# Optimization experiments

Hardware: AMD Instinct MI355X
Metric: run time of the kernel (lower is better)

The kernel has to match this reference:

```python
import jax, jax.numpy as jnp
import numpy as np

B, V, NL, D, H, DH, FS, CD, TL = 16, 8192, 12, 1024, 16, 64, 16, 768, 128
INNER, FF, SEQ = H * DH, 4 * D, FS * FS - 1  # 1024, 4096, 255
EPS = 1e-5


def _pos_indices(size):
    ar = np.arange(size)
    pos = np.stack(np.meshgrid(ar, ar, indexing='ij'), -1).reshape(-1, 2)  # (size^2, 2)
    rel = pos[:, None, :] - pos[None, :, :] + size - 1
    return jnp.asarray(rel[..., 0] * (2 * size - 1) + rel[..., 1])  # (size^2, size^2)


POS_IDX = _pos_indices(FS)


def _ln(x, g):
    mu = jnp.mean(x, -1, keepdims=True)
    var = jnp.mean(jnp.square(x - mu), -1, keepdims=True)
    return (x - mu) * jax.lax.rsqrt(var + EPS) * g


def _attn(x, ctx, g, Wq, nullkv, Wkv, Wout, og, pos_bias=None, ctx_mask=None, causal=False):
    b, n = x.shape[0], x.shape[1]
    xn = _ln(x, g)
    if ctx is None:
        ctx = xn  # self-attention: context is the normed input
    q = (xn @ Wq).reshape(b, n, H, DH).transpose(0, 2, 1, 3) * DH ** -0.5  # [b,h,n,dh]
    kv = ctx @ Wkv  # multi-query: single shared kv head [b,m,dh]
    kv = jnp.concatenate([jnp.broadcast_to(nullkv, (b, 1, DH)), kv], axis=1)  # null kv
    j = kv.shape[1]
    sim = jnp.einsum('bhid,bjd->bhij', q, kv)
    if pos_bias is not None:
        bias = pos_bias[POS_IDX[:n, :j - 1]]  # [n, j-1, h]
        sim = sim + jnp.pad(jnp.transpose(bias, (2, 0, 1)), ((0, 0), (0, 0), (1, 0)))
    big = jnp.finfo(sim.dtype).max
    if ctx_mask is not None:
        m = jnp.concatenate([jnp.ones((b, 1), bool), ctx_mask], axis=1)  # null kv never masked
        sim = jnp.where(m[:, None, None, :], sim, -big)
    if causal:
        cm = jnp.triu(jnp.ones((n, j), bool), k=j - n + 1)
        sim = jnp.where(cm, -big, sim)
    attn = jax.nn.softmax(sim.astype(jnp.float32), axis=-1).astype(sim.dtype)
    out = jnp.einsum('bhij,bjd->bhid', attn, kv).transpose(0, 2, 1, 3).reshape(b, n, INNER)
    return _ln(out @ Wout, og)


def setup_inputs() -> dict:
    key = jax.random.key(0)
    ks = iter(jax.random.split(key, 40))
    r = lambda *s: jax.random.normal(next(ks), s, jnp.float32) * 0.02
    return dict(
        image_token_ids=jax.random.randint(next(ks), (B, SEQ), 0, V),
        text_token_embeds=jax.random.normal(next(ks), (B, TL, CD), jnp.float32),
        text_mask=jnp.ones((B, TL), bool),
        tok_emb=r(V, D),
        axial_height_pos=r(FS, D),
        axial_width_pos=r(FS, D),
        start_token=r(D),
        init_gamma=jnp.ones(D, jnp.float32),
        sa_norm_g=jnp.ones((NL, D), jnp.float32), sa_Wq=r(NL, D, INNER), sa_null=r(NL, DH),
        sa_Wkv=r(NL, D, DH), sa_Wout=r(NL, INNER, D), sa_out_g=jnp.ones((NL, D), jnp.float32),
        sa_posbias=r(NL, (2 * FS - 1) ** 2, H),
        ca_norm_g=jnp.ones((NL, D), jnp.float32), ca_Wq=r(NL, D, INNER), ca_null=r(NL, DH),
        ca_Wkv=r(NL, CD, DH), ca_Wout=r(NL, INNER, D), ca_out_g=jnp.ones((NL, D), jnp.float32),
        ff_g1=jnp.ones((NL, D), jnp.float32), ff_W1=r(NL, D, FF),
        ff_g2=jnp.ones((NL, FF), jnp.float32), ff_W2=r(NL, FF, D),
        final_gamma=jnp.ones(D, jnp.float32),
    )


def reference(image_token_ids, text_token_embeds, text_mask, tok_emb, axial_height_pos,
              axial_width_pos, start_token, init_gamma, sa_norm_g, sa_Wq, sa_null, sa_Wkv,
              sa_Wout, sa_out_g, sa_posbias, ca_norm_g, ca_Wq, ca_null, ca_Wkv, ca_Wout,
              ca_out_g, ff_g1, ff_W1, ff_g2, ff_W2, final_gamma):
    b = image_token_ids.shape[0]
    emb = tok_emb[image_token_ids]  # [b, 255, D]
    axial = (axial_height_pos[:, None, :] + axial_width_pos[None, :, :]).reshape(-1, D)
    emb = emb + axial[:emb.shape[1]]
    x = jnp.concatenate([jnp.broadcast_to(start_token, (b, 1, D)), emb], axis=1)  # [b,256,D]
    # cond_drop_prob = 0: text_mask used as-is (deterministic)
    x = _ln(x, init_gamma)
    for l in range(NL):
        x = _attn(x, None, sa_norm_g[l], sa_Wq[l], sa_null[l], sa_Wkv[l], sa_Wout[l],
                  sa_out_g[l], pos_bias=sa_posbias[l], causal=True) + x
        x = _attn(x, text_token_embeds, ca_norm_g[l], ca_Wq[l], ca_null[l], ca_Wkv[l],
                  ca_Wout[l], ca_out_g[l], ctx_mask=text_mask) + x
        h = jax.nn.gelu(_ln(x, ff_g1[l]) @ ff_W1[l], approximate=False)
        x = _ln(h, ff_g2[l]) @ ff_W2[l] + x
    x = _ln(x, final_gamma)
    return x @ tok_emb.T  # tied embedding logits [b,256,V]
```

## Files before the change

kernel.cpp:

```cpp
#include <hip/hip_runtime.h>
#include <math.h>

typedef unsigned short u16;
typedef __attribute__((ext_vector_type(4))) unsigned short u16x4;
typedef __attribute__((ext_vector_type(8))) unsigned short u16x8;
typedef __attribute__((ext_vector_type(8))) short s16x8;
typedef __attribute__((ext_vector_type(4))) float f32x4;

#define DEV __device__ __forceinline__

DEV u16 f2bf(float f) {
  unsigned u = __float_as_uint(f);
  u += 0x7fffu + ((u >> 16) & 1u);
  return (u16)(u >> 16);
}
DEV float bf2f(u16 h) { return __uint_as_float(((unsigned)h) << 16); }

DEV void gload_lds16(const u16* g, u16* l) {
  __builtin_amdgcn_global_load_lds(
      (const __attribute__((address_space(1))) unsigned int*)(const void*)g,
      (__attribute__((address_space(3))) unsigned int*)(void*)l, 16, 0, 0);
}

template<int N> DEV void wait_vm() {
  if constexpr (N == 8)      asm volatile("s_waitcnt vmcnt(8)" ::: "memory");
  else if constexpr (N == 6) asm volatile("s_waitcnt vmcnt(6)" ::: "memory");
  else if constexpr (N == 4) asm volatile("s_waitcnt vmcnt(4)" ::: "memory");
  else                       asm volatile("s_waitcnt vmcnt(0)" ::: "memory");
}

DEV float block_sum256(float v, float* sb) {
  #pragma unroll
  for (int o = 32; o > 0; o >>= 1) v += __shfl_down(v, o);
  __syncthreads();
  if ((threadIdx.x & 63) == 0) sb[threadIdx.x >> 6] = v;
  __syncthreads();
  return sb[0] + sb[1] + sb[2] + sb[3];
}

__global__ __launch_bounds__(256) void wconv_t(const float* __restrict__ in, u16* __restrict__ outp,
                                               int R, int C, size_t ils, size_t ols, float sc) {
  __shared__ float tile[32][33];
  const float* inl = in + (size_t)blockIdx.z * ils;
  u16* outl = outp + (size_t)blockIdx.z * ols;
  int r0 = blockIdx.x * 32, c0 = blockIdx.y * 32;
  int tx = threadIdx.x, ty = threadIdx.y;
  #pragma unroll
  for (int i = ty; i < 32; i += 8)
    tile[i][tx] = inl[(size_t)(r0 + i) * C + (c0 + tx)];
  __syncthreads();
  #pragma unroll
  for (int i = ty; i < 32; i += 8)
    outl[(size_t)(c0 + i) * R + (r0 + tx)] = f2bf(tile[tx][i] * sc);
}

__global__ __launch_bounds__(256) void cvt_bf16_kernel(const float* __restrict__ in, u16* __restrict__ outp, size_t n) {
  size_t i = (size_t)blockIdx.x * blockDim.x + threadIdx.x;
  size_t stride = (size_t)gridDim.x * blockDim.x;
  for (; i < n; i += stride) outp[i] = f2bf(in[i]);
}

__global__ __launch_bounds__(256) void zfill16(u16* __restrict__ p, size_t lstride) {
  size_t o = (size_t)blockIdx.y * lstride + ((size_t)blockIdx.x * 256 + threadIdx.x) * 8;
  *(u16x8*)(p + o) = (u16x8){0, 0, 0, 0, 0, 0, 0, 0};
}

__global__ __launch_bounds__(256) void bias_tr(const float* __restrict__ pb, float* __restrict__ bt) {
  int l = blockIdx.x;
  for (int idx = threadIdx.x; idx < 961 * 16; idx += 256) {
    int p = idx >> 4, h = idx & 15;
    bt[((size_t)l * 16 + h) * 961 + p] = pb[(size_t)l * 15376 + idx];
  }
}

template<int BM, int BN, int WM, int WN, bool OUTBF>
__global__ __launch_bounds__(512, 2)
void gemm8(const u16* __restrict__ A, const u16* __restrict__ Bt, void* __restrict__ Cout,
           int M, int N, int K, int KS) {
  constexpr int BK = 64;
  constexpr int WROWS = BM / WM, WCOLS = BN / WN;
  constexpr int MR = WROWS / 16, NR = WCOLS / 16;
  constexpr int ABYTES = BM * BK * 2, BBYTES = BN * BK * 2;
  constexpr int TBYTES = ABYTES + BBYTES;
  constexpr int NCHA = ABYTES / 8192, NCHB = BBYTES / 8192;
  constexpr int LOADS = NCHA + NCHB;
  __shared__ char lds[2 * TBYTES];
  const int tid = threadIdx.x;
  const int lane = tid & 63;
  const int wave = tid >> 6;
  const int wr = wave / WN, wc = wave % WN;
  const int gX = gridDim.x;
  const int nwg = gX * gridDim.y;
  const int orig = blockIdx.y * gX + blockIdx.x;
  const int lin = (orig & 7) * (nwg >> 3) + (orig >> 3);
  const int bx = lin % gX, by = lin / gX;
  const size_t m0 = (size_t)bx * BM, n0 = (size_t)by * BN;
  const int k0 = blockIdx.z * KS;
  const size_t ldb = (size_t)K * 2;
  const char* Ab = (const char*)A + m0 * ldb + (size_t)k0 * 2;
  const char* Bb = (const char*)Bt + n0 * ldb + (size_t)k0 * 2;
  const int NT = KS / BK;

  auto stage = [&](int kt, char* buf) {
    const char* ga = Ab + kt * (BK * 2);
    #pragma unroll
    for (int c = 0; c < NCHA; ++c) {
      int d = (tid + c * 512) * 16;
      int o = d ^ (((d >> 9) & 1) << 5);
      gload_lds16((const u16*)(ga + (size_t)(o >> 7) * ldb + (o & 127)), (u16*)(buf + d));
    }
    const char* gb = Bb + kt * (BK * 2);
    #pragma unroll
    for (int c = 0; c < NCHB; ++c) {
      int d = (tid + c * 512) * 16;
      int o = d ^ (((d >> 9) & 1) << 5);
      gload_lds16((const u16*)(gb + (size_t)(o >> 7) * ldb + (o & 127)), (u16*)(buf + ABYTES + d));
    }
  };

  stage(0, lds);
  stage(1, lds + TBYTES);

  f32x4 acc[MR][NR];
  #pragma unroll
  for (int i = 0; i < MR; ++i)
    #pragma unroll
    for (int j = 0; j < NR; ++j) acc[i][j] = (f32x4){0.f, 0.f, 0.f, 0.f};

  const int rlane = lane & 15;
  const int glane = lane >> 4;
  const int swz = ((lane >> 2) & 1) << 5;

  for (int kt = 0; kt < NT; ++kt) {
    char* buf = lds + (kt & 1) * TBYTES;
    const char* At = buf;
    const char* Btl = buf + ABYTES;
    if (kt + 1 < NT) wait_vm<LOADS>(); else wait_vm<0>();
    asm volatile("s_barrier" ::: "memory");
    s16x8 bfr[NR][2];
    #pragma unroll
    for (int j = 0; j < NR; ++j)
      #pragma unroll
      for (int ks = 0; ks < 2; ++ks) {
        int o = ((wc * WCOLS + j * 16 + rlane) * 128 + ks * 64 + glane * 16) ^ swz;
        bfr[j][ks] = *(const s16x8*)(Btl + o);
      }
    #pragma unroll
    for (int mh = 0; mh < 2; ++mh) {
      s16x8 af[MR / 2][2];
      #pragma unroll
      for (int i = 0; i < MR / 2; ++i)
        #pragma unroll
        for (int ks = 0; ks < 2; ++ks) {
          int row = wr * WROWS + (mh * (MR / 2) + i) * 16 + rlane;
          int o = (row * 128 + ks * 64 + glane * 16) ^ swz;
          af[i][ks] = *(const s16x8*)(At + o);
        }
      __builtin_amdgcn_s_setprio(1);
      #pragma unroll
      for (int i = 0; i < MR / 2; ++i)
        #pragma unroll
        for (int j = 0; j < NR; ++j)
          #pragma unroll
          for (int ks = 0; ks < 2; ++ks)
            acc[mh * (MR / 2) + i][j] = __builtin_amdgcn_mfma_f32_16x16x32_bf16(
                af[i][ks], bfr[j][ks], acc[mh * (MR / 2) + i][j], 0, 0, 0);
      __builtin_amdgcn_s_setprio(0);
    }
    asm volatile("s_waitcnt lgkmcnt(0)\n\ts_barrier" ::: "memory");
    if (kt + 2 < NT) stage(kt + 2, buf);
  }

  char* Cb = (char*)Cout + (size_t)blockIdx.z * M * (size_t)N * (OUTBF ? 2 : 4);
  #pragma unroll
  for (int i = 0; i < MR; ++i)
    #pragma unroll
    for (int j = 0; j < NR; ++j) {
      size_t row = m0 + wr * WROWS + i * 16 + glane * 4;
      size_t col = n0 + wc * WCOLS + j * 16 + rlane;
      #pragma unroll
      for (int r = 0; r < 4; ++r) {
        size_t off = (row + r) * (size_t)N + col;
        if (OUTBF) ((u16*)Cb)[off] = f2bf(acc[i][j][r]);
        else       ((float*)Cb)[off] = acc[i][j][r];
      }
    }
}

template<bool OUTBF>
__global__ __launch_bounds__(256) void ln1024(const float* __restrict__ X, const float* __restrict__ g,
                                              float* Of, u16* Ob) {
  __shared__ float sb[4];
  size_t row = blockIdx.x;
  f32x4 v = *(const f32x4*)(X + row * 1024 + threadIdx.x * 4);
  float s = v[0] + v[1] + v[2] + v[3];
  float mu = block_sum256(s, sb) * (1.f / 1024.f);
  float q = 0.f;
  #pragma unroll
  for (int c = 0; c < 4; ++c) { float d = v[c] - mu; q += d * d; }
  float var = block_sum256(q, sb) * (1.f / 1024.f);
  float rs = rsqrtf(var + 1e-5f);
  f32x4 gg = *(const f32x4*)(g + threadIdx.x * 4);
  if (OUTBF) {
    u16x4 o;
    #pragma unroll
    for (int c = 0; c < 4; ++c) o[c] = f2bf((v[c] - mu) * rs * gg[c]);
    *(u16x4*)(Ob + row * 1024 + threadIdx.x * 4) = o;
  } else {
    f32x4 o;
    #pragma unroll
    for (int c = 0; c < 4; ++c) o[c] = (v[c] - mu) * rs * gg[c];
    *(f32x4*)(Of + row * 1024 + threadIdx.x * 4) = o;
  }
}

__global__ __launch_bounds__(256) void lnln_kernel(const float* __restrict__ T, const float* __restrict__ og,
                                                   const float* __restrict__ X, const float* __restrict__ g2,
                                                   float* __restrict__ Xn, u16* __restrict__ Ob) {
  __shared__ float sb[4];
  size_t row = blockIdx.x;
  size_t o4 = row * 1024 + threadIdx.x * 4;
  f32x4 v = *(const f32x4*)(T + o4);
  float s = v[0] + v[1] + v[2] + v[3];
  float mu = block_sum256(s, sb) * (1.f / 1024.f);
  float q = 0.f;
  #pragma unroll
  for (int c = 0; c < 4; ++c) { float d = v[c] - mu; q += d * d; }
  float var = block_sum256(q, sb) * (1.f / 1024.f);
  float rs = rsqrtf(var + 1e-5f);
  f32x4 ogv = *(const f32x4*)(og + threadIdx.x * 4);
  f32x4 xv  = *(const f32x4*)(X + o4);
  f32x4 u;
  #pragma unroll
  for (int c = 0; c < 4; ++c) u[c] = (v[c] - mu) * rs * ogv[c] + xv[c];
  *(f32x4*)(Xn + o4) = u;
  float s2 = u[0] + u[1] + u[2] + u[3];
  float mu2 = block_sum256(s2, sb) * (1.f / 1024.f);
  float q2 = 0.f;
  #pragma unroll
  for (int c = 0; c < 4; ++c) { float d = u[c] - mu2; q2 += d * d; }
  float var2 = block_sum256(q2, sb) * (1.f / 1024.f);
  float rs2 = rsqrtf(var2 + 1e-5f);
  f32x4 g2v = *(const f32x4*)(g2 + threadIdx.x * 4);
  u16x4 ob;
  #pragma unroll
  for (int c = 0; c < 4; ++c) ob[c] = f2bf((u[c] - mu2) * rs2 * g2v[c]);
  *(u16x4*)(Ob + o4) = ob;
}

__global__ __launch_bounds__(256) void addln_kernel(const float* __restrict__ X, const float* __restrict__ P0,
                                                    const float* __restrict__ g,
                                                    float* __restrict__ Xn, u16* __restrict__ Ob) {
  __shared__ float sb[4];
  size_t row = blockIdx.x;
  size_t o4 = row * 1024 + threadIdx.x * 4;
  f32x4 a = *(const f32x4*)(X + o4);
  f32x4 p = *(const f32x4*)(P0 + o4);
  f32x4 v;
  #pragma unroll
  for (int c = 0; c < 4; ++c) v[c] = a[c] + p[c];
  *(f32x4*)(Xn + o4) = v;
  float s = v[0] + v[1] + v[2] + v[3];
  float mu = block_sum256(s, sb) * (1.f / 1024.f);
  float q = 0.f;
  #pragma unroll
  for (int c = 0; c < 4; ++c) { float d = v[c] - mu; q += d * d; }
  float var = block_sum256(q, sb) * (1.f / 1024.f);
  float rs = rsqrtf(var + 1e-5f);
  f32x4 gg = *(const f32x4*)(g + threadIdx.x * 4);
  u16x4 ob;
  #pragma unroll
  for (int c = 0; c < 4; ++c) ob[c] = f2bf((v[c] - mu) * rs * gg[c]);
  *(u16x4*)(Ob + o4) = ob;
}

__global__ __launch_bounds__(256) void gelu_ln_bf(const u16* __restrict__ T, const float* __restrict__ g,
                                                  u16* __restrict__ Ob) {
  __shared__ float sb[4];
  size_t row = blockIdx.x;
  size_t o16 = row * 4096 + threadIdx.x * 16;
  u16x8 t0 = *(const u16x8*)(T + o16);
  u16x8 t1 = *(const u16x8*)(T + o16 + 8);
  float v[16];
  #pragma unroll
  for (int c = 0; c < 8; ++c) {
    float a = bf2f(t0[c]);
    v[c] = 0.5f * a * (1.f + erff(a * 0.70710678118654752f));
    float b = bf2f(t1[c]);
    v[c + 8] = 0.5f * b * (1.f + erff(b * 0.70710678118654752f));
  }
  float s = 0.f;
  #pragma unroll
  for (int c = 0; c < 16; ++c) s += v[c];
  float mu = block_sum256(s, sb) * (1.f / 4096.f);
  float q = 0.f;
  #pragma unroll
  for (int c = 0; c < 16; ++c) { float d = v[c] - mu; q += d * d; }
  float var = block_sum256(q, sb) * (1.f / 4096.f);
  float rs = rsqrtf(var + 1e-5f);
  u16x8 o0, o1;
  #pragma unroll
  for (int c = 0; c < 8; ++c) {
    o0[c] = f2bf((v[c] - mu) * rs * g[threadIdx.x * 16 + c]);
    o1[c] = f2bf((v[c + 8] - mu) * rs * g[threadIdx.x * 16 + 8 + c]);
  }
  *(u16x8*)(Ob + o16) = o0;
  *(u16x8*)(Ob + o16 + 8) = o1;
}

__global__ __launch_bounds__(256) void embed_ln_kernel(const int* __restrict__ ids, const float* __restrict__ tok,
                                                       const float* __restrict__ hpos, const float* __restrict__ wpos,
                                                       const float* __restrict__ start, const float* __restrict__ gamma,
                                                       float* __restrict__ X) {
  __shared__ float sb[4];
  int p = blockIdx.x, b = blockIdx.y;
  float v[4];
  if (p == 0) {
    #pragma unroll
    for (int c = 0; c < 4; ++c) v[c] = start[threadIdx.x + c * 256];
  } else {
    int s = p - 1;
    int id = ids[b * 255 + s];
    #pragma unroll
    for (int c = 0; c < 4; ++c) {
      int col = threadIdx.x + c * 256;
      v[c] = tok[(size_t)id * 1024 + col] + hpos[(s >> 4) * 1024 + col] + wpos[(s & 15) * 1024 + col];
    }
  }
  float s0 = 0.f;
  #pragma unroll
  for (int c = 0; c < 4; ++c) s0 += v[c];
  float mu = block_sum256(s0, sb) * (1.f / 1024.f);
  float q = 0.f;
  #pragma unroll
  for (int c = 0; c < 4; ++c) { float d = v[c] - mu; q += d * d; }
  float var = block_sum256(q, sb) * (1.f / 1024.f);
  float rs = rsqrtf(var + 1e-5f);
  #pragma unroll
  for (int c = 0; c < 4; ++c) {
    int col = threadIdx.x + c * 256;
    X[((size_t)b * 256 + p) * 1024 + col] = (v[c] - mu) * rs * gamma[col];
  }
}

__global__ __launch_bounds__(256) void kv_build_sa(const u16* __restrict__ qkv, const float* __restrict__ nul,
                                                   u16* __restrict__ kv, u16* __restrict__ kvT) {
  constexpr int JP = 288, J = 257;
  int b = blockIdx.x;
  for (int idx = threadIdx.x; idx < JP * 64; idx += 256) {
    int j = idx >> 6, d = idx & 63;
    u16 hv = 0;
    if (j == 0) hv = f2bf(nul[d]);
    else if (j < J) hv = qkv[(size_t)(b * 256 + j - 1) * 1152 + 1024 + d];
    kv[((size_t)b * JP + j) * 64 + d] = hv;
    kvT[((size_t)b * 64 + d) * JP + j] = hv;
  }
}

__global__ __launch_bounds__(256) void kv_build_ca(const u16* __restrict__ src, int sstride, int scol,
                                                   const float* __restrict__ nul,
                                                   u16* __restrict__ kv, u16* __restrict__ kvT) {
  constexpr int JP = 160, J = 129;
  int b = blockIdx.x, l = blockIdx.y;
  for (int idx = threadIdx.x; idx < JP * 64; idx += 256) {
    int j = idx >> 6, d = idx & 63;
    u16 hv = 0;
    if (j == 0) hv = f2bf(nul[l * 64 + d]);
    else if (j < J) hv = src[(size_t)(b * 128 + j - 1) * sstride + l * scol + d];
    kv[(((size_t)l * 16 + b) * JP + j) * 64 + d] = hv;
    kvT[(((size_t)l * 16 + b) * 64 + d) * JP + j] = hv;
  }
}

template<int NJT, int KSP, bool CAUSAL, bool BIAS>
__global__ __launch_bounds__(256) void attn_mfma(const u16* __restrict__ Q, int QS,
                                                 const u16* __restrict__ kvb, const u16* __restrict__ kvTb,
                                                 const float* __restrict__ bias, u16* __restrict__ O, int J) {
  constexpr int JP = KSP * 32;
  constexpr int PSTR = KSP * 32 + 16;
  __shared__ __align__(16) u16 Plds[4][16][PSTR];
  const int lane = threadIdx.x & 63, wave = threadIdx.x >> 6;
  const int h = blockIdx.y, b = blockIdx.z;
  const int i0 = blockIdx.x * 64 + wave * 16;
  const int c = lane & 15, g = lane >> 4;
  const float* biasrow = BIAS ? (bias + (size_t)h * 961) : nullptr;

  s16x8 aq[2];
  #pragma unroll
  for (int ks = 0; ks < 2; ++ks)
    aq[ks] = *(const s16x8*)(Q + (size_t)(b * 256 + i0 + c) * QS + h * 64 + ks * 32 + g * 8);

  f32x4 acc[NJT];
  #pragma unroll
  for (int jt = 0; jt < NJT; ++jt) acc[jt] = (f32x4){0.f, 0.f, 0.f, 0.f};

  const u16* kvB = kvb + (size_t)b * JP * 64;
  __builtin_amdgcn_s_setprio(1);
  #pragma unroll
  for (int ks = 0; ks < 2; ++ks) {
    #pragma unroll
    for (int jt = 0; jt < NJT; ++jt) {
      s16x8 bf = *(const s16x8*)(kvB + (size_t)(jt * 16 + c) * 64 + ks * 32 + g * 8);
      acc[jt] = __builtin_amdgcn_mfma_f32_16x16x32_bf16(aq[ks], bf, acc[jt], 0, 0, 0);
    }
  }
  __builtin_amdgcn_s_setprio(0);

  const float NEGINF = -__builtin_inff();
  #pragma unroll
  for (int r = 0; r < 4; ++r) {
    const int i = i0 + g * 4 + r;
    float mx = NEGINF;
    #pragma unroll
    for (int jt = 0; jt < NJT; ++jt) {
      int j = jt * 16 + c;
      float s = acc[jt][r];
      if (j >= J) s = NEGINF;
      else {
        if (BIAS && j >= 1) {
          int t = j - 1;
          int idx = ((i >> 4) - (t >> 4) + 15) * 31 + ((i & 15) - (t & 15) + 15);
          s += biasrow[idx];
        }
        if (CAUSAL && j > i + 1) s = NEGINF;
      }
      acc[jt][r] = s;
      mx = fmaxf(mx, s);
    }
    #pragma unroll
    for (int o = 1; o < 16; o <<= 1) mx = fmaxf(mx, __shfl_xor(mx, o));
    float sum = 0.f;
    #pragma unroll
    for (int jt = 0; jt < NJT; ++jt) {
      float p = __expf(acc[jt][r] - mx);
      acc[jt][r] = p;
      sum += p;
    }
    #pragma unroll
    for (int o = 1; o < 16; o <<= 1) sum += __shfl_xor(sum, o);
    float inv = 1.f / sum;
    #pragma unroll
    for (int jt = 0; jt < NJT; ++jt)
      Plds[wave][g * 4 + r][jt * 16 + c] = f2bf(acc[jt][r] * inv);
  }
  #pragma unroll
  for (int z = 0; z < 4; ++z)
    Plds[wave][c][NJT * 16 + g * 4 + z] = 0;

  s16x8 pa[KSP];
  #pragma unroll
  for (int ks = 0; ks < KSP; ++ks)
    pa[ks] = *(const s16x8*)(&Plds[wave][c][ks * 32 + g * 8]);
  const u16* kvT = kvTb + (size_t)b * 64 * JP;
  #pragma unroll
  for (int nt = 0; nt < 4; ++nt) {
    f32x4 ov = (f32x4){0.f, 0.f, 0.f, 0.f};
    __builtin_amdgcn_s_setprio(1);
    #pragma unroll
    for (int ks = 0; ks < KSP; ++ks) {
      s16x8 bv = *(const s16x8*)(kvT + (size_t)(nt * 16 + c) * JP + ks * 32 + g * 8);
      ov = __builtin_amdgcn_mfma_f32_16x16x32_bf16(pa[ks], bv, ov, 0, 0, 0);
    }
    __builtin_amdgcn_s_setprio(0);
    #pragma unroll
    for (int r = 0; r < 4; ++r)
      O[(size_t)(b * 256 + i0 + g * 4 + r) * 1024 + h * 64 + nt * 16 + c] = f2bf(ov[r]);
  }
}

extern "C" void kernel_launch(void* const* d_in, const int* in_sizes, int n_in,
                              void* d_out, int out_size, void* d_ws, size_t ws_size,
                              hipStream_t stream) {
  const int*   ids     = (const int*)  d_in[0];
  const float* text    = (const float*)d_in[1];
  const float* tok     = (const float*)d_in[3];
  const float* hpos    = (const float*)d_in[4];
  const float* wpos    = (const float*)d_in[5];
  const float* start   = (const float*)d_in[6];
  const float* initg   = (const float*)d_in[7];
  const float* sa_g    = (const float*)d_in[8];
  const float* sa_Wq   = (const float*)d_in[9];
  const float* sa_nul  = (const float*)d_in[10];
  const float* sa_Wkv  = (const float*)d_in[11];
  const float* sa_Wout = (const float*)d_in[12];
  const float* sa_og   = (const float*)d_in[13];
  const float* sa_pb   = (const float*)d_in[14];
  const float* ca_g    = (const float*)d_in[15];
  const float* ca_Wq   = (const float*)d_in[16];
  const float* ca_nul  = (const float*)d_in[17];
  const float* ca_Wkv  = (const float*)d_in[18];
  const float* ca_Wout = (const float*)d_in[19];
  const float* ca_og   = (const float*)d_in[20];
  const float* ff_g1   = (const float*)d_in[21];
  const float* ff_W1   = (const float*)d_in[22];
  const float* ff_g2   = (const float*)d_in[23];
  const float* ff_W2   = (const float*)d_in[24];
  const float* fing    = (const float*)d_in[25];
  float* out = (float*)d_out;

  char* base = (char*)d_ws;
  size_t off = 0;
  auto carve = [&](size_t bytes) -> char* {
    off = (off + 255) & ~(size_t)255;
    char* p = base + off;
    off += bytes;
    return p;
  };
  float* x       = (float*)carve(4096ull * 1024 * 4);
  float* t       = (float*)carve(4096ull * 4096 * 4);
  u16*   xn      = (u16*)  carve(4096ull * 1024 * 2);
  u16*   qkv     = (u16*)  carve(4096ull * 1152 * 2);
  u16*   qb      = (u16*)  carve(4096ull * 1024 * 2);
  u16*   ao      = (u16*)  carve(4096ull * 1024 * 2);
  u16*   hb      = (u16*)  carve(4096ull * 4096 * 2);
  u16*   kvbuf   = (u16*)  carve(16ull * 288 * 64 * 2);
  u16*   kvTbuf  = (u16*)  carve(16ull * 64 * 288 * 2);
  u16*   cakv    = (u16*)  carve(12ull * 16 * 160 * 64 * 2);
  u16*   cakvT   = (u16*)  carve(12ull * 16 * 64 * 160 * 2);
  u16*   catmp   = (u16*)  carve(2048ull * 768 * 2);
  u16*   cakvw   = (u16*)  carve(12ull * 64 * 768 * 2);
  u16*   cakvw1  = (u16*)  carve(128ull * 768 * 2);
  u16*   catmp1  = (u16*)  carve(2048ull * 128 * 2);
  u16*   textbf  = (u16*)  carve(2048ull * 768 * 2);
  u16*   tokbf   = (u16*)  carve(8192ull * 1024 * 2);
  float* biast   = (float*)carve(12ull * 16 * 961 * 4);
  u16*   tb      = (u16*)t;

  const size_t O_WQKV = 0;
  const size_t O_WOUT = 1179648;
  const size_t O_CWQ  = 2228224;
  const size_t O_CWOUT= 3276800;
  const size_t O_W1   = 4325376;
  const size_t O_W2   = 8519680;
  const size_t LAYER_E = 12713984ull;
  size_t off_now = (off + 255) & ~(size_t)255;
  bool allw = (off_now + 12 * LAYER_E * 2) <= ws_size;
  u16* wbase = (u16*)carve((allw ? 12 : 1) * LAYER_E * 2);

  dim3 tb8(32, 8);
  auto conv = [&](const float* in, u16* op, int R, int C, int L, float sc) {
    wconv_t<<<dim3(R / 32, C / 32, L), tb8, 0, stream>>>(in, op, R, C, (size_t)R * C, LAYER_E, sc);
  };
  if (allw) {
    conv(sa_Wq,   wbase + O_WQKV,            1024, 1024, 12, 0.125f);
    conv(sa_Wkv,  wbase + O_WQKV + 1048576,  1024, 64,   12, 1.f);
    zfill16<<<dim3(32, 12), 256, 0, stream>>>(wbase + O_WQKV + 1114112, LAYER_E);
    conv(sa_Wout, wbase + O_WOUT,  1024, 1024, 12, 1.f);
    conv(ca_Wq,   wbase + O_CWQ,   1024, 1024, 12, 0.125f);
    conv(ca_Wout, wbase + O_CWOUT, 1024, 1024, 12, 1.f);
    conv(ff_W1,   wbase + O_W1,    1024, 4096, 12, 1.f);
    conv(ff_W2,   wbase + O_W2,    4096, 1024, 12, 1.f);
    wconv_t<<<dim3(24, 2, 12), tb8, 0, stream>>>(ca_Wkv, cakvw, 768, 64, 49152, 49152, 1.f);
  }
  bias_tr<<<12, 256, 0, stream>>>(sa_pb, biast);
  cvt_bf16_kernel<<<2048, 256, 0, stream>>>(tok, tokbf, 8192ull * 1024);
  cvt_bf16_kernel<<<1024, 256, 0, stream>>>(text, textbf, 2048ull * 768);
  if (allw) {
    gemm8<128, 128, 2, 4, true><<<dim3(16, 6, 1), 512, 0, stream>>>(textbf, cakvw, catmp, 2048, 768, 768, 768);
    kv_build_ca<<<dim3(16, 12), 256, 0, stream>>>(catmp, 768, 64, ca_nul, cakv, cakvT);
  }
  embed_ln_kernel<<<dim3(256, 16), 256, 0, stream>>>(ids, tok, hpos, wpos, start, initg, x);
  ln1024<true><<<4096, 256, 0, stream>>>(x, sa_g, nullptr, xn);

  for (int l = 0; l < 12; ++l) {
    u16* W = allw ? (wbase + (size_t)l * LAYER_E) : wbase;
    if (!allw) {
      conv(sa_Wq   + (size_t)l * 1048576, W + O_WQKV,           1024, 1024, 1, 0.125f);
      conv(sa_Wkv  + (size_t)l * 65536,   W + O_WQKV + 1048576, 1024, 64,   1, 1.f);
      zfill16<<<dim3(32, 1), 256, 0, stream>>>(W + O_WQKV + 1114112, 0);
      conv(sa_Wout + (size_t)l * 1048576, W + O_WOUT,  1024, 1024, 1, 1.f);
      conv(ca_Wq   + (size_t)l * 1048576, W + O_CWQ,   1024, 1024, 1, 0.125f);
      conv(ca_Wout + (size_t)l * 1048576, W + O_CWOUT, 1024, 1024, 1, 1.f);
      conv(ff_W1   + (size_t)l * 4194304, W + O_W1,    1024, 4096, 1, 1.f);
      conv(ff_W2   + (size_t)l * 4194304, W + O_W2,    4096, 1024, 1, 1.f);
      wconv_t<<<dim3(24, 2, 1), tb8, 0, stream>>>(ca_Wkv + (size_t)l * 49152, cakvw1, 768, 64, 0, 0, 1.f);
      zfill16<<<dim3(24, 1), 256, 0, stream>>>(cakvw1 + 64 * 768, 0);
      gemm8<128, 128, 2, 4, true><<<dim3(16, 1, 1), 512, 0, stream>>>(textbf, cakvw1, catmp1, 2048, 128, 768, 768);
      kv_build_ca<<<dim3(16, 1), 256, 0, stream>>>(catmp1, 128, 0, ca_nul + l * 64,
                                                   cakv + (size_t)l * 16 * 160 * 64,
                                                   cakvT + (size_t)l * 16 * 64 * 160);
    }
    gemm8<128, 128, 2, 4, true><<<dim3(32, 9, 1), 512, 0, stream>>>(xn, W + O_WQKV, qkv, 4096, 1152, 1024, 1024);
    kv_build_sa<<<16, 256, 0, stream>>>(qkv, sa_nul + l * 64, kvbuf, kvTbuf);
    attn_mfma<17, 9, true, true><<<dim3(4, 16, 16), 256, 0, stream>>>(qkv, 1152, kvbuf, kvTbuf,
                                                                      biast + (size_t)l * 16 * 961, ao, 257);
    gemm8<128, 128, 2, 4, false><<<dim3(32, 8, 1), 512, 0, stream>>>(ao, W + O_WOUT, t, 4096, 1024, 1024, 1024);
    lnln_kernel<<<4096, 256, 0, stream>>>(t, sa_og + l * 1024, x, ca_g + l * 1024, x, xn);
    gemm8<128, 128, 2, 4, true><<<dim3(32, 8, 1), 512, 0, stream>>>(xn, W + O_CWQ, qb, 4096, 1024, 1024, 1024);
    attn_mfma<9, 5, false, false><<<dim3(4, 16, 16), 256, 0, stream>>>(qb, 1024,
                                                                       cakv + (size_t)l * 16 * 160 * 64,
                                                                       cakvT + (size_t)l * 16 * 64 * 160,
                                                                       nullptr, ao, 129);
    gemm8<128, 128, 2, 4, false><<<dim3(32, 8, 1), 512, 0, stream>>>(ao, W + O_CWOUT, t, 4096, 1024, 1024, 1024);
    lnln_kernel<<<4096, 256, 0, stream>>>(t, ca_og + l * 1024, x, ff_g1 + l * 1024, x, xn);
    gemm8<256, 256, 2, 4, true><<<dim3(16, 16, 1), 512, 0, stream>>>(xn, W + O_W1, tb, 4096, 4096, 1024, 1024);
    gelu_ln_bf<<<4096, 256, 0, stream>>>(tb, ff_g2 + (size_t)l * 4096, hb);
    gemm8<128, 128, 2, 4, false><<<dim3(32, 8, 1), 512, 0, stream>>>(hb, W + O_W2, t, 4096, 1024, 4096, 4096);
    addln_kernel<<<4096, 256, 0, stream>>>(x, t, (l < 11 ? sa_g + (l + 1) * 1024 : fing), x, xn);
  }
  gemm8<256, 256, 2, 4, false><<<dim3(16, 32, 1), 512, 0, stream>>>(xn, tokbf, out, 4096, 8192, 1024, 1024);
}
```

Measured before the change: 4.383 ms.

## Fuse self-attention KV build into QKV GEMM epilogue and shrink N=1024 GEMM tiles

Removes the separate kv_build_sa kernel by having the QKV GEMM epilogue write the shared K/V column block directly into the padded kv and transposed kvT buffers, with one wave per batch writing the null-kv row. The padding is zero-filled once up front. Separately, the N=1024 projection GEMMs switch from 128x128 to 64x128 tiles, doubling the grid from 256 to 512 workgroups for better CU fill. The smaller tiles reduce per-workgroup data reuse, and the epilogue gains scattered strided kvT stores.

```diff
diff --git a/kernel.cpp b/kernel.cpp
--- a/kernel.cpp
+++ b/kernel.cpp
@@ -26,6 +26,7 @@
   if constexpr (N == 8)      asm volatile("s_waitcnt vmcnt(8)" ::: "memory");
   else if constexpr (N == 6) asm volatile("s_waitcnt vmcnt(6)" ::: "memory");
   else if constexpr (N == 4) asm volatile("s_waitcnt vmcnt(4)" ::: "memory");
+  else if constexpr (N == 3) asm volatile("s_waitcnt vmcnt(3)" ::: "memory");
   else                       asm volatile("s_waitcnt vmcnt(0)" ::: "memory");
 }
 
@@ -73,10 +74,11 @@
   }
 }
 
-template<int BM, int BN, int WM, int WN, bool OUTBF>
+template<int BM, int BN, int WM, int WN, bool OUTBF, bool KV>
 __global__ __launch_bounds__(512, 2)
 void gemm8(const u16* __restrict__ A, const u16* __restrict__ Bt, void* __restrict__ Cout,
-           int M, int N, int K, int KS) {
+           int M, int N, int K, int KS,
+           const float* __restrict__ nul, u16* __restrict__ kv, u16* __restrict__ kvT) {
   constexpr int BK = 64;
   constexpr int WROWS = BM / WM, WCOLS = BN / WN;
   constexpr int MR = WROWS / 16, NR = WCOLS / 16;
@@ -181,10 +183,29 @@
       #pragma unroll
       for (int r = 0; r < 4; ++r) {
         size_t off = (row + r) * (size_t)N + col;
-        if (OUTBF) ((u16*)Cb)[off] = f2bf(acc[i][j][r]);
-        else       ((float*)Cb)[off] = acc[i][j][r];
+        float v = acc[i][j][r];
+        if (OUTBF) ((u16*)Cb)[off] = f2bf(v);
+        else       ((float*)Cb)[off] = v;
+        if (KV) {
+          if (col >= (size_t)(N - 128) && col < (size_t)(N - 64)) {
+            int d = (int)(col - (N - 128));
+            int b = (int)((row + r) >> 8);
+            int jj = (int)((row + r) & 255) + 1;
+            u16 hv = f2bf(v);
+            kv[((size_t)b * 288 + jj) * 64 + d] = hv;
+            kvT[((size_t)b * 64 + d) * 288 + jj] = hv;
+          }
+        }
       }
     }
+  if (KV) {
+    if ((bx & 3) == 0 && (int)n0 == N - 128 && wave == 0) {
+      int b = bx >> 2;
+      u16 hv = f2bf(nul[lane]);
+      kv[(size_t)b * 288 * 64 + lane] = hv;
+      kvT[((size_t)b * 64 + lane) * 288] = hv;
+    }
+  }
 }
 
 template<bool OUTBF>
@@ -340,20 +361,6 @@
   for (int c = 0; c < 4; ++c) {
     int col = threadIdx.x + c * 256;
     X[((size_t)b * 256 + p) * 1024 + col] = (v[c] - mu) * rs * gamma[col];
-  }
-}
-
-__global__ __launch_bounds__(256) void kv_build_sa(const u16* __restrict__ qkv, const float* __restrict__ nul,
-                                                   u16* __restrict__ kv, u16* __restrict__ kvT) {
-  constexpr int JP = 288, J = 257;
-  int b = blockIdx.x;
-  for (int idx = threadIdx.x; idx < JP * 64; idx += 256) {
-    int j = idx >> 6, d = idx & 63;
-    u16 hv = 0;
-    if (j == 0) hv = f2bf(nul[d]);
-    else if (j < J) hv = qkv[(size_t)(b * 256 + j - 1) * 1152 + 1024 + d];
-    kv[((size_t)b * JP + j) * 64 + d] = hv;
-    kvT[((size_t)b * 64 + d) * JP + j] = hv;
   }
 }
 
@@ -372,11 +379,10 @@
   }
 }
 
-template<int NJT, int KSP, bool CAUSAL, bool BIAS>
+template<int NJT, int KSP, int JPT, bool CAUSAL, bool BIAS>
 __global__ __launch_bounds__(256) void attn_mfma(const u16* __restrict__ Q, int QS,
                                                  const u16* __restrict__ kvb, const u16* __restrict__ kvTb,
                                                  const float* __restrict__ bias, u16* __restrict__ O, int J) {
-  constexpr int JP = KSP * 32;
   constexpr int PSTR = KSP * 32 + 16;
   __shared__ __align__(16) u16 Plds[4][16][PSTR];
   const int lane = threadIdx.x & 63, wave = threadIdx.x >> 6;
@@ -394,7 +400,7 @@
   #pragma unroll
   for (int jt = 0; jt < NJT; ++jt) acc[jt] = (f32x4){0.f, 0.f, 0.f, 0.f};
 
-  const u16* kvB = kvb + (size_t)b * JP * 64;
+  const u16* kvB = kvb + (size_t)b * JPT * 64;
   __builtin_amdgcn_s_setprio(1);
   #pragma unroll
   for (int ks = 0; ks < 2; ++ks) {
@@ -451,14 +457,14 @@
   #pragma unroll
   for (int ks = 0; ks < KSP; ++ks)
     pa[ks] = *(const s16x8*)(&Plds[wave][c][ks * 32 + g * 8]);
-  const u16* kvT = kvTb + (size_t)b * 64 * JP;
+  const u16* kvT = kvTb + (size_t)b * 64 * JPT;
   #pragma unroll
   for (int nt = 0; nt < 4; ++nt) {
     f32x4 ov = (f32x4){0.f, 0.f, 0.f, 0.f};
     __builtin_amdgcn_s_setprio(1);
     #pragma unroll
     for (int ks = 0; ks < KSP; ++ks) {
-      s16x8 bv = *(const s16x8*)(kvT + (size_t)(nt * 16 + c) * JP + ks * 32 + g * 8);
+      s16x8 bv = *(const s16x8*)(kvT + (size_t)(nt * 16 + c) * JPT + ks * 32 + g * 8);
       ov = __builtin_amdgcn_mfma_f32_16x16x32_bf16(pa[ks], bv, ov, 0, 0, 0);
     }
     __builtin_amdgcn_s_setprio(0);
@@ -524,7 +530,7 @@
   u16*   textbf  = (u16*)  carve(2048ull * 768 * 2);
   u16*   tokbf   = (u16*)  carve(8192ull * 1024 * 2);
   float* biast   = (float*)carve(12ull * 16 * 961 * 4);
-  u16*   tb      = (u16*)t;
+  u16*   tbb     = (u16*)t;
 
   const size_t O_WQKV = 0;
   const size_t O_WOUT = 1179648;
@@ -553,10 +559,12 @@
     wconv_t<<<dim3(24, 2, 12), tb8, 0, stream>>>(ca_Wkv, cakvw, 768, 64, 49152, 49152, 1.f);
   }
   bias_tr<<<12, 256, 0, stream>>>(sa_pb, biast);
+  zfill16<<<dim3(144, 1), 256, 0, stream>>>(kvbuf, 0);
+  zfill16<<<dim3(144, 1), 256, 0, stream>>>(kvTbuf, 0);
   cvt_bf16_kernel<<<2048, 256, 0, stream>>>(tok, tokbf, 8192ull * 1024);
   cvt_bf16_kernel<<<1024, 256, 0, stream>>>(text, textbf, 2048ull * 768);
   if (allw) {
-    gemm8<128, 128, 2, 4, true><<<dim3(16, 6, 1), 512, 0, stream>>>(textbf, cakvw, catmp, 2048, 768, 768, 768);
+    gemm8<128, 128, 2, 4, true, false><<<dim3(16, 6, 1), 512, 0, stream>>>(textbf, cakvw, catmp, 2048, 768, 768, 768, nullptr, nullptr, nullptr);
     kv_build_ca<<<dim3(16, 12), 256, 0, stream>>>(catmp, 768, 64, ca_nul, cakv, cakvT);
   }
   embed_ln_kernel<<<dim3(256, 16), 256, 0, stream>>>(ids, tok, hpos, wpos, start, initg, x);
@@ -575,28 +583,28 @@
       conv(ff_W2   + (size_t)l * 4194304, W + O_W2,    4096, 1024, 1, 1.f);
       wconv_t<<<dim3(24, 2, 1), tb8, 0, stream>>>(ca_Wkv + (size_t)l * 49152, cakvw1, 768, 64, 0, 0, 1.f);
       zfill16<<<dim3(24, 1), 256, 0, stream>>>(cakvw1 + 64 * 768, 0);
-      gemm8<128, 128, 2, 4, true><<<dim3(16, 1, 1), 512, 0, stream>>>(textbf, cakvw1, catmp1, 2048, 128, 768, 768);
+      gemm8<128, 128, 2, 4, true, false><<<dim3(16, 1, 1), 512, 0, stream>>>(textbf, cakvw1, catmp1, 2048, 128, 768, 768, nullptr, nullptr, nullptr);
       kv_build_ca<<<dim3(16, 1), 256, 0, stream>>>(catmp1, 128, 0, ca_nul + l * 64,
                                                    cakv + (size_t)l * 16 * 160 * 64,
                                                    cakvT + (size_t)l * 16 * 64 * 160);
     }
-    gemm8<128, 128, 2, 4, true><<<dim3(32, 9, 1), 512, 0, stream>>>(xn, W + O_WQKV, qkv, 4096, 1152, 1024, 1024);
-    kv_build_sa<<<16, 256, 0, stream>>>(qkv, sa_nul + l * 64, kvbuf, kvTbuf);
-    attn_mfma<17, 9, true, true><<<dim3(4, 16, 16), 256, 0, stream>>>(qkv, 1152, kvbuf, kvTbuf,
-                                                                      biast + (size_t)l * 16 * 961, ao, 257);
-    gemm8<128, 128, 2, 4, false><<<dim3(32, 8, 1), 512, 0, stream>>>(ao, W + O_WOUT, t, 4096, 1024, 1024, 1024);
+    gemm8<64, 128, 2, 4, true, true><<<dim3(64, 9, 1), 512, 0, stream>>>(xn, W + O_WQKV, qkv, 4096, 1152, 1024, 1024,
+                                                                         sa_nul + l * 64, kvbuf, kvTbuf);
+    attn_mfma<17, 9, 288, true, true><<<dim3(4, 16, 16), 256, 0, stream>>>(qkv, 1152, kvbuf, kvTbuf,
+                                                                           biast + (size_t)l * 16 * 961, ao, 257);
+    gemm8<64, 128, 2, 4, false, false><<<dim3(64, 8, 1), 512, 0, stream>>>(ao, W + O_WOUT, t, 4096, 1024, 1024, 1024, nullptr, nullptr, nullptr);
     lnln_kernel<<<4096, 256, 0, stream>>>(t, sa_og + l * 1024, x, ca_g + l * 1024, x, xn);
-    gemm8<128, 128, 2, 4, true><<<dim3(32, 8, 1), 512, 0, stream>>>(xn, W + O_CWQ, qb, 4096, 1024, 1024, 1024);
-    attn_mfma<9, 5, false, false><<<dim3(4, 16, 16), 256, 0, stream>>>(qb, 1024,
-                                                                       cakv + (size_t)l * 16 * 160 * 64,
-                                                                       cakvT + (size_t)l * 16 * 64 * 160,
-                                                                       nullptr, ao, 129);
-    gemm8<128, 128, 2, 4, false><<<dim3(32, 8, 1), 512, 0, stream>>>(ao, W + O_CWOUT, t, 4096, 1024, 1024, 1024);
+    gemm8<64, 128, 2, 4, true, false><<<dim3(64, 8, 1), 512, 0, stream>>>(xn, W + O_CWQ, qb, 4096, 1024, 1024, 1024, nullptr, nullptr, nullptr);
+    attn_mfma<9, 5, 160, false, false><<<dim3(4, 16, 16), 256, 0, stream>>>(qb, 1024,
+                                                                            cakv + (size_t)l * 16 * 160 * 64,
+                                                                            cakvT + (size_t)l * 16 * 64 * 160,
+                                                                            nullptr, ao, 129);
+    gemm8<64, 128, 2, 4, false, false><<<dim3(64, 8, 1), 512, 0, stream>>>(ao, W + O_CWOUT, t, 4096, 1024, 1024, 1024, nullptr, nullptr, nullptr);
     lnln_kernel<<<4096, 256, 0, stream>>>(t, ca_og + l * 1024, x, ff_g1 + l * 1024, x, xn);
-    gemm8<256, 256, 2, 4, true><<<dim3(16, 16, 1), 512, 0, stream>>>(xn, W + O_W1, tb, 4096, 4096, 1024, 1024);
-    gelu_ln_bf<<<4096, 256, 0, stream>>>(tb, ff_g2 + (size_t)l * 4096, hb);
-    gemm8<128, 128, 2, 4, false><<<dim3(32, 8, 1), 512, 0, stream>>>(hb, W + O_W2, t, 4096, 1024, 4096, 4096);
+    gemm8<256, 256, 2, 4, true, false><<<dim3(16, 16, 1), 512, 0, stream>>>(xn, W + O_W1, tbb, 4096, 4096, 1024, 1024, nullptr, nullptr, nullptr);
+    gelu_ln_bf<<<4096, 256, 0, stream>>>(tbb, ff_g2 + (size_t)l * 4096, hb);
+    gemm8<64, 128, 2, 4, false, false><<<dim3(64, 8, 1), 512, 0, stream>>>(hb, W + O_W2, t, 4096, 1024, 4096, 4096, nullptr, nullptr, nullptr);
     addln_kernel<<<4096, 256, 0, stream>>>(x, t, (l < 11 ? sa_g + (l + 1) * 1024 : fing), x, xn);
   }
-  gemm8<256, 256, 2, 4, false><<<dim3(16, 32, 1), 512, 0, stream>>>(xn, tokbf, out, 4096, 8192, 1024, 1024);
-}
+  gemm8<256, 256, 2, 4, false, false><<<dim3(16, 32, 1), 512, 0, stream>>>(xn, tokbf, out, 4096, 8192, 1024, 1024, nullptr, nullptr, nullptr);
+}
```

After: 4.077 ms. 7.0% less time.
